# Optimization experiments

Measured on AMD Instinct MI355X. Metric: run time of the kernel, lower is better.

The kernel has to match this reference:

```python
import jax, jax.numpy as jnp
import numpy as np

# dims matching init_kwargs
E = 256        # obs dim
H = 128        # rnn_hidden_dim
NQ = 8         # n_quantiles (forward_type='policy')
QED = 64       # quantile_embed_dim
HEADS = 2      # hpn_head_num
HYP = 64       # hpn_hyper_dim
NA = 14        # n_actions
NAG = 8        # n_agents
B = 512        # episode batch


def setup_inputs() -> dict:
    key = jax.random.key(0)
    ks = jax.random.split(key, 16)
    def rn(k, shape, scale):
        return jax.random.normal(k, shape, dtype=jnp.float32) * scale
    inp = {
        "inputs": rn(ks[0], (B, NAG, E), 1.0),
        "hidden_state": rn(ks[1], (B * NAG, H), 1.0),
        "rnd_quantiles": jax.random.uniform(ks[2], (B, 1, NQ), dtype=jnp.float32),
        # fc1
        "fc1_w": rn(ks[3], (E, H), 1.0 / np.sqrt(E)),
        "fc1_b": jnp.zeros((H,), jnp.float32),
        # hypernet (2-layer MLP producing per-sample H x (H*HEADS) weights)
        "hyp_w1": rn(ks[4], (NQ, HYP), 1.0 / np.sqrt(NQ)),
        "hyp_b1": jnp.zeros((HYP,), jnp.float32),
        "hyp_w2": rn(ks[5], (HYP, H * H * HEADS), 1.0 / np.sqrt(HYP)),
        "hyp_b2": jnp.zeros((H * H * HEADS,), jnp.float32),
        # merger softmax weights [1, heads, H], init 1.0 as in module
        "merger_w": jnp.ones((1, HEADS, H), jnp.float32),
        # GRUCell params (PyTorch layout: [3H, in])
        "gru_wi": rn(ks[6], (3 * H, H), 1.0 / np.sqrt(H)),
        "gru_wh": rn(ks[7], (3 * H, H), 1.0 / np.sqrt(H)),
        "gru_bi": jnp.zeros((3 * H,), jnp.float32),
        "gru_bh": jnp.zeros((3 * H,), jnp.float32),
        # phi (quantile embedding linear)
        "phi_w": rn(ks[8], (QED, H), 1.0 / np.sqrt(QED)),
        "phi_b": jnp.zeros((H,), jnp.float32),
        # fc2
        "fc2_w": rn(ks[9], (H, NA), 1.0 / np.sqrt(H)),
        "fc2_b": jnp.zeros((NA,), jnp.float32),
    }
    return inp


def reference(inputs, hidden_state, rnd_quantiles, fc1_w, fc1_b,
              hyp_w1, hyp_b1, hyp_w2, hyp_b2, merger_w,
              gru_wi, gru_wh, gru_bi, gru_bh, phi_w, phi_b, fc2_w, fc2_b):
    b, a, e = inputs.shape
    bs = b * a
    # fc1 + relu
    x = jax.nn.relu(inputs.reshape(bs, e) @ fc1_w + fc1_b)          # [bs, H]
    # prev return distribution: first-call value = ones
    prev = jnp.ones((bs, NQ), dtype=inputs.dtype)
    # hypernet -> per-sample weights [bs, H, H*HEADS]
    hh = jax.nn.relu(prev @ hyp_w1 + hyp_b1)
    input_w = (hh @ hyp_w2 + hyp_b2).reshape(bs, H, H * HEADS)
    # batched matmul: [bs,1,H] @ [bs,H,H*HEADS] -> [bs, HEADS, H]
    emb = jnp.einsum('bi,bio->bo', x, input_w).reshape(bs, HEADS, H)
    # merger: softmax over head dim
    emb = jnp.sum(jax.nn.softmax(merger_w, axis=1) * emb, axis=1)   # [bs, H]
    x2 = jax.nn.relu(emb)
    # GRUCell (PyTorch semantics)
    hprev = hidden_state.reshape(-1, H)
    gi = x2 @ gru_wi.T + gru_bi
    gh = hprev @ gru_wh.T + gru_bh
    ir, iz, inn = jnp.split(gi, 3, axis=1)
    hr, hz, hn = jnp.split(gh, 3, axis=1)
    r = jax.nn.sigmoid(ir + hr)
    z = jax.nn.sigmoid(iz + hz)
    n = jnp.tanh(inn + r * hn)
    h = (1.0 - z) * n + z * hprev                                   # [bs, H]
    # IQN quantile embedding (forward_type='policy', grouped by agents)
    nq = NQ
    bsg = bs // NAG
    rq = rnd_quantiles.reshape(-1)                                  # [bsg*nq]
    h2 = jnp.broadcast_to(h[:, None, :], (bs, nq, H)).reshape(bs * nq, H)
    fid = jnp.arange(QED, dtype=inputs.dtype)                       # [QED]
    cos = jnp.cos(jnp.pi * fid[None, :] * rq[:, None])              # [bsg*nq, QED]
    q_phi = jax.nn.relu(cos @ phi_w + phi_b)                        # [bsg*nq, H]
    q_phi = jnp.broadcast_to(q_phi.reshape(bsg, 1, nq, H),
                             (bsg, NAG, nq, H)).reshape(bs * nq, H)
    q = (h2 * q_phi) @ fc2_w + fc2_b                                # [bs*nq, NA]
    q = q.reshape(bs, nq, NA).transpose(0, 2, 1)                    # [bs, NA, nq]
    sorted_q = jnp.sort(q, axis=2)
    return sorted_q, h, rq.reshape(bsg, nq)
```

## Files before the change

kernel.cpp:

```cpp
#include <hip/hip_runtime.h>
#include <math.h>

typedef __attribute__((ext_vector_type(8))) short short8;
typedef __attribute__((ext_vector_type(4))) float floatx4;

#define E_DIM 256
#define H_DIM 128
#define NQv 8
#define QEDv 64
#define HYPv 64
#define NAv 14
#define NAGv 8
#define W2COL 32768

#define OUT_H_OFF 458752
#define OUT_RQ_OFF 983040

#define FB_W1  0
#define FB_WE  4096
#define FB_WI  6144
#define FB_WH  12288
#define FB_PHI 18432
#define FB_FC2 19456
#define PACK_UNITS 17664
#define PACK_BLOCKS 69
#define WEFF_BLOCKS 256

#define SM_IN   0
#define SM_X1   8192
#define SM_X2   12288
#define SM_H    16384
#define SM_PART 0
#define SM_HF   32768
#define SM_QP   41216
#define SM_TOTAL 45568

__device__ __forceinline__ unsigned short f2bf(float x) {
  unsigned u = __builtin_bit_cast(unsigned, x);
  u += 0x7FFFu + ((u >> 16) & 1u);
  return (unsigned short)(u >> 16);
}
__device__ __forceinline__ float bf2f(unsigned short s) {
  return __builtin_bit_cast(float, ((unsigned)s) << 16);
}
__device__ __forceinline__ float fsigmoid(float x) {
  return 1.f / (1.f + __expf(-x));
}
__device__ __forceinline__ float ftanh(float x) {
  float t = __expf(-2.f * x);
  return (1.f - t) / (1.f + t);
}

__global__ __launch_bounds__(256) void k_prep(
    const float* __restrict__ fc1_w, const float* __restrict__ gru_wi,
    const float* __restrict__ gru_wh, const float* __restrict__ phi_w,
    const float* __restrict__ fc2_w,
    const float* __restrict__ hyp_w1, const float* __restrict__ hyp_b1,
    const float* __restrict__ hyp_w2, const float* __restrict__ hyp_b2,
    const float* __restrict__ merger_w, unsigned short* __restrict__ wp) {
  __shared__ float hh[HYPv];
  __shared__ float part[4][2][64];
  int t = threadIdx.x;

  if (blockIdx.x < PACK_BLOCKS) {
    int u = blockIdx.x * 256 + t;
    if (u >= PACK_UNITS) return;
    float v[8];
    int f;
    if (u < 4096) {
      int g = u, nt = (g >> 6) & 7, lane = g & 63;
      int k0 = (g >> 9) * 32 + ((lane >> 4) << 3), n = nt * 16 + (lane & 15);
      f = FB_W1 + g;
#pragma unroll
      for (int j = 0; j < 8; ++j) v[j] = fc1_w[(k0 + j) * H_DIM + n];
    } else if (u < 10240) {
      int g = u - 4096, kt = g / 1536, rem = g % 1536, nt = rem >> 6, lane = rem & 63;
      int k0 = kt * 32 + ((lane >> 4) << 3), n = nt * 16 + (lane & 15);
      f = FB_WI + g;
#pragma unroll
      for (int j = 0; j < 8; ++j) v[j] = gru_wi[n * H_DIM + k0 + j];
    } else if (u < 16384) {
      int g = u - 10240, kt = g / 1536, rem = g % 1536, nt = rem >> 6, lane = rem & 63;
      int k0 = kt * 32 + ((lane >> 4) << 3), n = nt * 16 + (lane & 15);
      f = FB_WH + g;
#pragma unroll
      for (int j = 0; j < 8; ++j) v[j] = gru_wh[n * H_DIM + k0 + j];
    } else if (u < 17408) {
      int g = u - 16384, kt = g >> 9, nt = (g >> 6) & 7, lane = g & 63;
      int k0 = kt * 32 + ((lane >> 4) << 3), n = nt * 16 + (lane & 15);
      f = FB_PHI + g;
#pragma unroll
      for (int j = 0; j < 8; ++j) v[j] = phi_w[(k0 + j) * H_DIM + n];
    } else {
      int g = u - 17408, kt = g >> 6, lane = g & 63;
      int k0 = kt * 32 + ((lane >> 4) << 3), n = lane & 15;
      f = FB_FC2 + g;
#pragma unroll
      for (int j = 0; j < 8; ++j) v[j] = (n < NAv) ? fc2_w[(k0 + j) * NAv + n] : 0.f;
    }
    short8 pk;
#pragma unroll
    for (int j = 0; j < 8; ++j) pk[j] = (short)f2bf(v[j]);
    *(short8*)(wp + (size_t)f * 8) = pk;
    return;
  }

  int blk = blockIdx.x - PACK_BLOCKS;
  if (t < HYPv) {
    float s = hyp_b1[t];
#pragma unroll
    for (int i = 0; i < NQv; ++i) s += hyp_w1[i * HYPv + t];
    hh[t] = fmaxf(s, 0.f);
  }
  __syncthreads();
  int w = t >> 6, lane = t & 63;
  int i = blk >> 1;
  int cbase = (blk & 1) * 64;
  int o0 = i * 256 + cbase + lane;
  float a0 = 0.f, a1 = 0.f;
#pragma unroll
  for (int jj = 0; jj < 16; ++jj) {
    int j = w * 16 + jj;
    float hj = hh[j];
    a0 = fmaf(hj, hyp_w2[j * W2COL + o0], a0);
    a1 = fmaf(hj, hyp_w2[j * W2COL + o0 + 128], a1);
  }
  part[w][0][lane] = a0;
  part[w][1][lane] = a1;
  __syncthreads();
  if (t < 64) {
    int c = cbase + t;
    float h0 = part[0][0][t] + part[1][0][t] + part[2][0][t] + part[3][0][t]
               + hyp_b2[i * 256 + c];
    float h1 = part[0][1][t] + part[1][1][t] + part[2][1][t] + part[3][1][t]
               + hyp_b2[i * 256 + c + 128];
    float m0 = merger_w[c], m1 = merger_w[128 + c];
    float mx = fmaxf(m0, m1);
    float e0 = expf(m0 - mx), e1 = expf(m1 - mx);
    float val = (e0 * h0 + e1 * h1) / (e0 + e1);
    int unit = FB_WE + ((i >> 5) * 8 + (c >> 4)) * 64 + ((i >> 3) & 3) * 16 + (c & 15);
    wp[(size_t)unit * 8 + (i & 7)] = f2bf(val);
  }
}

__global__ __launch_bounds__(256) void k_main(
    const float* __restrict__ inp, const float* __restrict__ hprev,
    const float* __restrict__ rnd, const float* __restrict__ fc1_b,
    const unsigned short* __restrict__ wp,
    const float* __restrict__ gru_bi, const float* __restrict__ gru_bh,
    const float* __restrict__ phi_b, const float* __restrict__ fc2_b,
    float* __restrict__ h_out, float* __restrict__ q_out,
    float* __restrict__ rq_out) {
  __shared__ __align__(16) char smem[SM_TOTAL];
  unsigned short (*lds_in)[64][8] = (unsigned short(*)[64][8])(smem + SM_IN);
  unsigned short (*lds_x1)[64][8] = (unsigned short(*)[64][8])(smem + SM_X1);
  unsigned short (*lds_x2)[64][8] = (unsigned short(*)[64][8])(smem + SM_X2);
  unsigned short (*lds_h)[64][8]  = (unsigned short(*)[64][8])(smem + SM_H);
  float (*lds_hf)[132]            = (float(*)[132])(smem + SM_HF);
  unsigned short (*lds_qp)[136]   = (unsigned short(*)[136])(smem + SM_QP);
  float* lds_part                 = (float*)(smem + SM_PART);

  int t = threadIdx.x;
  int b0 = blockIdx.x * 16;
  int lane = t & 63, w = t >> 6;
  int quad = lane >> 4, l16 = lane & 15;
  int nt0 = w * 2;

  short8 bPhi[2][2], bW1[8][2], bWE[4][2];
#pragma unroll
  for (int kt = 0; kt < 2; ++kt)
#pragma unroll
    for (int ni = 0; ni < 2; ++ni)
      bPhi[kt][ni] = *(const short8*)(wp +
          ((size_t)(FB_PHI + (kt * 8 + nt0 + ni) * 64 + lane)) * 8);
#pragma unroll
  for (int kt = 0; kt < 8; ++kt)
#pragma unroll
    for (int ni = 0; ni < 2; ++ni)
      bW1[kt][ni] = *(const short8*)(wp +
          ((size_t)(FB_W1 + (kt * 8 + nt0 + ni) * 64 + lane)) * 8);
#pragma unroll
  for (int kt = 0; kt < 4; ++kt)
#pragma unroll
    for (int ni = 0; ni < 2; ++ni)
      bWE[kt][ni] = *(const short8*)(wp +
          ((size_t)(FB_WE + (kt * 8 + nt0 + ni) * 64 + lane)) * 8);

  if (t < 16) rq_out[b0 + t] = rnd[b0 + t];

#pragma unroll
  for (int i = 0; i < 2; ++i) {
    int idx = i * 256 + t;
    int oct = idx & 31, m = idx >> 5;
    const float* p = inp + (size_t)(b0 + m) * E_DIM + oct * 8;
    floatx4 v0 = *(const floatx4*)p;
    floatx4 v1 = *(const floatx4*)(p + 4);
    short8 pk;
    pk[0] = (short)f2bf(v0.x); pk[1] = (short)f2bf(v0.y);
    pk[2] = (short)f2bf(v0.z); pk[3] = (short)f2bf(v0.w);
    pk[4] = (short)f2bf(v1.x); pk[5] = (short)f2bf(v1.y);
    pk[6] = (short)f2bf(v1.z); pk[7] = (short)f2bf(v1.w);
    *(short8*)&lds_in[oct >> 2][(oct & 3) * 16 + m][0] = pk;
  }
  {
    int oct = t & 15, m = t >> 4;
    const float* p = hprev + (size_t)(b0 + m) * H_DIM + oct * 8;
    floatx4 v0 = *(const floatx4*)p;
    floatx4 v1 = *(const floatx4*)(p + 4);
    short8 pk;
    pk[0] = (short)f2bf(v0.x); pk[1] = (short)f2bf(v0.y);
    pk[2] = (short)f2bf(v0.z); pk[3] = (short)f2bf(v0.w);
    pk[4] = (short)f2bf(v1.x); pk[5] = (short)f2bf(v1.y);
    pk[6] = (short)f2bf(v1.z); pk[7] = (short)f2bf(v1.w);
    *(short8*)&lds_h[oct >> 2][(oct & 3) * 16 + m][0] = pk;
  }

  {
    float rqv = rnd[b0 + l16];
    short8 aC[2];
#pragma unroll
    for (int kt = 0; kt < 2; ++kt) {
#pragma unroll
      for (int j = 0; j < 8; ++j) {
        float f = (float)(kt * 32 + quad * 8 + j);
        aC[kt][j] = (short)f2bf(__cosf(3.14159265358979f * f * rqv));
      }
    }
    floatx4 cP[2] = {{0.f,0.f,0.f,0.f},{0.f,0.f,0.f,0.f}};
#pragma unroll
    for (int kt = 0; kt < 2; ++kt)
#pragma unroll
      for (int ni = 0; ni < 2; ++ni)
        cP[ni] = __builtin_amdgcn_mfma_f32_16x16x32_bf16(aC[kt], bPhi[kt][ni], cP[ni], 0, 0, 0);
#pragma unroll
    for (int ni = 0; ni < 2; ++ni) {
      int col = (nt0 + ni) * 16 + l16;
      float bias = phi_b[col];
#pragma unroll
      for (int reg = 0; reg < 4; ++reg) {
        int m_qp = quad * 4 + reg;
        lds_qp[m_qp][col] = f2bf(fmaxf(cP[ni][reg] + bias, 0.f));
      }
    }
  }
  __syncthreads();

  {
    short8 aIn[8];
#pragma unroll
    for (int kt = 0; kt < 8; ++kt)
      aIn[kt] = *(const short8*)&lds_in[kt][lane][0];
    floatx4 c1[2] = {{0.f,0.f,0.f,0.f},{0.f,0.f,0.f,0.f}};
#pragma unroll
    for (int kt = 0; kt < 8; ++kt)
#pragma unroll
      for (int n = 0; n < 2; ++n)
        c1[n] = __builtin_amdgcn_mfma_f32_16x16x32_bf16(aIn[kt], bW1[kt][n], c1[n], 0, 0, 0);
#pragma unroll
    for (int n = 0; n < 2; ++n) {
      int col = (nt0 + n) * 16 + l16;
      float bias = fc1_b[col];
#pragma unroll
      for (int reg = 0; reg < 4; ++reg) {
        float v = fmaxf(c1[n][reg] + bias, 0.f);
        lds_x1[col >> 5][((col >> 3) & 3) * 16 + quad * 4 + reg][col & 7] = f2bf(v);
      }
    }
  }
  __syncthreads();

  {
    short8 a2[4];
#pragma unroll
    for (int kt = 0; kt < 4; ++kt)
      a2[kt] = *(const short8*)&lds_x1[kt][lane][0];
    floatx4 c2[2] = {{0.f,0.f,0.f,0.f},{0.f,0.f,0.f,0.f}};
#pragma unroll
    for (int kt = 0; kt < 4; ++kt)
#pragma unroll
      for (int n = 0; n < 2; ++n)
        c2[n] = __builtin_amdgcn_mfma_f32_16x16x32_bf16(a2[kt], bWE[kt][n], c2[n], 0, 0, 0);
#pragma unroll
    for (int n = 0; n < 2; ++n) {
      int col = (nt0 + n) * 16 + l16;
#pragma unroll
      for (int reg = 0; reg < 4; ++reg) {
        float v = fmaxf(c2[n][reg], 0.f);
        lds_x2[col >> 5][((col >> 3) & 3) * 16 + quad * 4 + reg][col & 7] = f2bf(v);
      }
    }
  }
  __syncthreads();

  {
    short8 ax[4], ah[4];
#pragma unroll
    for (int kt = 0; kt < 4; ++kt) {
      ax[kt] = *(const short8*)&lds_x2[kt][lane][0];
      ah[kt] = *(const short8*)&lds_h[kt][lane][0];
    }
#pragma unroll
    for (int cti = 0; cti < 2; ++cti) {
      int ct = w + cti * 4;
      floatx4 giR = {0.f,0.f,0.f,0.f}, giZ = {0.f,0.f,0.f,0.f}, giN = {0.f,0.f,0.f,0.f};
      floatx4 ghR = {0.f,0.f,0.f,0.f}, ghZ = {0.f,0.f,0.f,0.f}, ghN = {0.f,0.f,0.f,0.f};
#pragma unroll
      for (int kt = 0; kt < 4; ++kt) {
        short8 bR = *(const short8*)(wp + ((size_t)(FB_WI + (kt * 24 + ct) * 64 + lane)) * 8);
        short8 bZ = *(const short8*)(wp + ((size_t)(FB_WI + (kt * 24 + ct + 8) * 64 + lane)) * 8);
        short8 bN = *(const short8*)(wp + ((size_t)(FB_WI + (kt * 24 + ct + 16) * 64 + lane)) * 8);
        short8 cR = *(const short8*)(wp + ((size_t)(FB_WH + (kt * 24 + ct) * 64 + lane)) * 8);
        short8 cZ = *(const short8*)(wp + ((size_t)(FB_WH + (kt * 24 + ct + 8) * 64 + lane)) * 8);
        short8 cN = *(const short8*)(wp + ((size_t)(FB_WH + (kt * 24 + ct + 16) * 64 + lane)) * 8);
        giR = __builtin_amdgcn_mfma_f32_16x16x32_bf16(ax[kt], bR, giR, 0, 0, 0);
        giZ = __builtin_amdgcn_mfma_f32_16x16x32_bf16(ax[kt], bZ, giZ, 0, 0, 0);
        giN = __builtin_amdgcn_mfma_f32_16x16x32_bf16(ax[kt], bN, giN, 0, 0, 0);
        ghR = __builtin_amdgcn_mfma_f32_16x16x32_bf16(ah[kt], cR, ghR, 0, 0, 0);
        ghZ = __builtin_amdgcn_mfma_f32_16x16x32_bf16(ah[kt], cZ, ghZ, 0, 0, 0);
        ghN = __builtin_amdgcn_mfma_f32_16x16x32_bf16(ah[kt], cN, ghN, 0, 0, 0);
      }
      int c = ct * 16 + l16;
      float bir = gru_bi[c], biz = gru_bi[128 + c], bin = gru_bi[256 + c];
      float bhr = gru_bh[c], bhz = gru_bh[128 + c], bhn = gru_bh[256 + c];
#pragma unroll
      for (int reg = 0; reg < 4; ++reg) {
        int rl = quad * 4 + reg;
        int row = b0 + rl;
        float r = fsigmoid(giR[reg] + bir + ghR[reg] + bhr);
        float z = fsigmoid(giZ[reg] + biz + ghZ[reg] + bhz);
        float n = ftanh(giN[reg] + bin + r * (ghN[reg] + bhn));
        float hp = hprev[(size_t)row * H_DIM + c];
        float hv = (1.f - z) * n + z * hp;
        h_out[(size_t)row * H_DIM + c] = hv;
        lds_hf[rl][c] = hv;
      }
    }
  }
  __syncthreads();

  {
    int m = l16;
    int k0 = w * 32 + quad * 8;
    const float* hptr = &lds_hf[m][k0];
    floatx4 h0 = *(const floatx4*)hptr;
    floatx4 h1 = *(const floatx4*)(hptr + 4);
    float hf[8] = {h0.x, h0.y, h0.z, h0.w, h1.x, h1.y, h1.z, h1.w};
    short8 bF = *(const short8*)(wp + ((size_t)(FB_FC2 + w * 64 + lane)) * 8);
    int qbase = (m >> 3) * 8;
    floatx4 cQ[8];
#pragma unroll
    for (int q = 0; q < NQv; ++q) cQ[q] = (floatx4){0.f,0.f,0.f,0.f};
#pragma unroll
    for (int q = 0; q < NQv; ++q) {
      short8 qpv = *(const short8*)&lds_qp[qbase + q][k0];
      short8 au;
#pragma unroll
      for (int j = 0; j < 8; ++j)
        au[j] = (short)f2bf(hf[j] * bf2f((unsigned short)qpv[j]));
      cQ[q] = __builtin_amdgcn_mfma_f32_16x16x32_bf16(au, bF, cQ[q], 0, 0, 0);
    }
#pragma unroll
    for (int q = 0; q < NQv; ++q)
      *(floatx4*)&lds_part[((w * 8 + q) * 64 + lane) * 4] = cQ[q];
  }
  __syncthreads();

  {
    int s = t >> 4, a = t & 15;
    int pl = (s >> 2) * 16 + a;
    int pr = s & 3;
    float bias = (a < NAv) ? fc2_b[a] : 0.f;
    float qv[NQv];
#pragma unroll
    for (int q = 0; q < NQv; ++q) {
      float acc = bias;
#pragma unroll
      for (int ww = 0; ww < 4; ++ww)
        acc += lds_part[((ww * 8 + q) * 64 + pl) * 4 + pr];
      qv[q] = acc;
    }
#define CE(i, j) { float lo_ = fminf(qv[i], qv[j]); float hi_ = fmaxf(qv[i], qv[j]); qv[i] = lo_; qv[j] = hi_; }
    CE(0,1) CE(2,3) CE(4,5) CE(6,7)
    CE(0,2) CE(1,3) CE(4,6) CE(5,7)
    CE(1,2) CE(5,6)
    CE(0,4) CE(1,5) CE(2,6) CE(3,7)
    CE(2,4) CE(3,5)
    CE(1,2) CE(3,4) CE(5,6)
#undef CE
    if (a < NAv) {
      float4* o4 = (float4*)(q_out + (size_t)((b0 + s) * NAv + a) * NQv);
      o4[0] = make_float4(qv[0], qv[1], qv[2], qv[3]);
      o4[1] = make_float4(qv[4], qv[5], qv[6], qv[7]);
    }
  }
}

extern "C" void kernel_launch(void* const* d_in, const int* in_sizes, int n_in,
                              void* d_out, int out_size, void* d_ws, size_t ws_size,
                              hipStream_t stream) {
  (void)in_sizes; (void)n_in; (void)out_size; (void)ws_size;
  const float* inp      = (const float*)d_in[0];
  const float* hidden   = (const float*)d_in[1];
  const float* rnd      = (const float*)d_in[2];
  const float* fc1_w    = (const float*)d_in[3];
  const float* fc1_b    = (const float*)d_in[4];
  const float* hyp_w1   = (const float*)d_in[5];
  const float* hyp_b1   = (const float*)d_in[6];
  const float* hyp_w2   = (const float*)d_in[7];
  const float* hyp_b2   = (const float*)d_in[8];
  const float* merger_w = (const float*)d_in[9];
  const float* gru_wi   = (const float*)d_in[10];
  const float* gru_wh   = (const float*)d_in[11];
  const float* gru_bi   = (const float*)d_in[12];
  const float* gru_bh   = (const float*)d_in[13];
  const float* phi_w    = (const float*)d_in[14];
  const float* phi_b    = (const float*)d_in[15];
  const float* fc2_w    = (const float*)d_in[16];
  const float* fc2_b    = (const float*)d_in[17];
  float* out  = (float*)d_out;
  unsigned short* wp = (unsigned short*)d_ws;
  float* h_out = out + OUT_H_OFF;

  k_prep<<<dim3(PACK_BLOCKS + WEFF_BLOCKS), dim3(256), 0, stream>>>(
      fc1_w, gru_wi, gru_wh, phi_w, fc2_w,
      hyp_w1, hyp_b1, hyp_w2, hyp_b2, merger_w, wp);
  k_main<<<dim3(256), dim3(256), 0, stream>>>(inp, hidden, rnd, fc1_b, wp,
                                              gru_bi, gru_bh, phi_b, fc2_b,
                                              h_out, out, out + OUT_RQ_OFF);
}
```

Before: 107.2 us.

## Remap GRU column tiles per wave, drop barrier, prefetch GRU and fc2 weights

GRU output column tiles are reassigned so each wave computes the 32 h columns it later reads in the fc2/quantile stage. That makes the __syncthreads between those stages unnecessary, so it is removed. The partial-sum LDS buffer is moved so it no longer aliases earlier buffers, which grows shared memory to about 66KB. The first GRU tile's weights are prefetched into registers before the x2 matmul, and the fc2 weight fragment is loaded at kernel start. The cost is more VGPR pressure and more LDS per block, which can lower occupancy.

```diff
diff --git a/kernel.cpp b/kernel.cpp
--- a/kernel.cpp
+++ b/kernel.cpp
@@ -30,10 +30,10 @@
 #define SM_X1   8192
 #define SM_X2   12288
 #define SM_H    16384
-#define SM_PART 0
-#define SM_HF   32768
-#define SM_QP   41216
-#define SM_TOTAL 45568
+#define SM_HF   20480
+#define SM_QP   28928
+#define SM_PART 33280
+#define SM_TOTAL 66048
 
 __device__ __forceinline__ unsigned short f2bf(float x) {
   unsigned u = __builtin_bit_cast(unsigned, x);
@@ -166,7 +166,7 @@
   int quad = lane >> 4, l16 = lane & 15;
   int nt0 = w * 2;
 
-  short8 bPhi[2][2], bW1[8][2], bWE[4][2];
+  short8 bPhi[2][2], bW1[8][2], bWE[4][2], bF;
 #pragma unroll
   for (int kt = 0; kt < 2; ++kt)
 #pragma unroll
@@ -185,6 +185,7 @@
     for (int ni = 0; ni < 2; ++ni)
       bWE[kt][ni] = *(const short8*)(wp +
           ((size_t)(FB_WE + (kt * 8 + nt0 + ni) * 64 + lane)) * 8);
+  bF = *(const short8*)(wp + ((size_t)(FB_FC2 + w * 64 + lane)) * 8);
 
   if (t < 16) rq_out[b0 + t] = rnd[b0 + t];
 
@@ -269,6 +270,19 @@
   }
   __syncthreads();
 
+  short8 pGi[4][3], pGh[4][3];
+  {
+    int ct = 2 * w;
+#pragma unroll
+    for (int kt = 0; kt < 4; ++kt) {
+#pragma unroll
+      for (int g = 0; g < 3; ++g) {
+        pGi[kt][g] = *(const short8*)(wp + ((size_t)(FB_WI + (kt * 24 + ct + g * 8) * 64 + lane)) * 8);
+        pGh[kt][g] = *(const short8*)(wp + ((size_t)(FB_WH + (kt * 24 + ct + g * 8) * 64 + lane)) * 8);
+      }
+    }
+  }
+
   {
     short8 a2[4];
 #pragma unroll
@@ -301,17 +315,23 @@
     }
 #pragma unroll
     for (int cti = 0; cti < 2; ++cti) {
-      int ct = w + cti * 4;
+      int ct = 2 * w + cti;
       floatx4 giR = {0.f,0.f,0.f,0.f}, giZ = {0.f,0.f,0.f,0.f}, giN = {0.f,0.f,0.f,0.f};
       floatx4 ghR = {0.f,0.f,0.f,0.f}, ghZ = {0.f,0.f,0.f,0.f}, ghN = {0.f,0.f,0.f,0.f};
 #pragma unroll
       for (int kt = 0; kt < 4; ++kt) {
-        short8 bR = *(const short8*)(wp + ((size_t)(FB_WI + (kt * 24 + ct) * 64 + lane)) * 8);
-        short8 bZ = *(const short8*)(wp + ((size_t)(FB_WI + (kt * 24 + ct + 8) * 64 + lane)) * 8);
-        short8 bN = *(const short8*)(wp + ((size_t)(FB_WI + (kt * 24 + ct + 16) * 64 + lane)) * 8);
-        short8 cR = *(const short8*)(wp + ((size_t)(FB_WH + (kt * 24 + ct) * 64 + lane)) * 8);
-        short8 cZ = *(const short8*)(wp + ((size_t)(FB_WH + (kt * 24 + ct + 8) * 64 + lane)) * 8);
-        short8 cN = *(const short8*)(wp + ((size_t)(FB_WH + (kt * 24 + ct + 16) * 64 + lane)) * 8);
+        short8 bR, bZ, bN, cR, cZ, cN;
+        if (cti == 0) {
+          bR = pGi[kt][0]; bZ = pGi[kt][1]; bN = pGi[kt][2];
+          cR = pGh[kt][0]; cZ = pGh[kt][1]; cN = pGh[kt][2];
+        } else {
+          bR = *(const short8*)(wp + ((size_t)(FB_WI + (kt * 24 + ct) * 64 + lane)) * 8);
+          bZ = *(const short8*)(wp + ((size_t)(FB_WI + (kt * 24 + ct + 8) * 64 + lane)) * 8);
+          bN = *(const short8*)(wp + ((size_t)(FB_WI + (kt * 24 + ct + 16) * 64 + lane)) * 8);
+          cR = *(const short8*)(wp + ((size_t)(FB_WH + (kt * 24 + ct) * 64 + lane)) * 8);
+          cZ = *(const short8*)(wp + ((size_t)(FB_WH + (kt * 24 + ct + 8) * 64 + lane)) * 8);
+          cN = *(const short8*)(wp + ((size_t)(FB_WH + (kt * 24 + ct + 16) * 64 + lane)) * 8);
+        }
         giR = __builtin_amdgcn_mfma_f32_16x16x32_bf16(ax[kt], bR, giR, 0, 0, 0);
         giZ = __builtin_amdgcn_mfma_f32_16x16x32_bf16(ax[kt], bZ, giZ, 0, 0, 0);
         giN = __builtin_amdgcn_mfma_f32_16x16x32_bf16(ax[kt], bN, giN, 0, 0, 0);
@@ -336,7 +356,6 @@
       }
     }
   }
-  __syncthreads();
 
   {
     int m = l16;
@@ -345,7 +364,6 @@
     floatx4 h0 = *(const floatx4*)hptr;
     floatx4 h1 = *(const floatx4*)(hptr + 4);
     float hf[8] = {h0.x, h0.y, h0.z, h0.w, h1.x, h1.y, h1.z, h1.w};
-    short8 bF = *(const short8*)(wp + ((size_t)(FB_FC2 + w * 64 + lane)) * 8);
     int qbase = (m >> 3) * 8;
     floatx4 cQ[8];
 #pragma unroll
```

After: 104.9 us. 2.1% less time.
